# Kernel optimization log

Hardware: AMD Instinct MI355X
Metric: run time of the kernel (lower is better)

## Reference

```python
import jax, jax.numpy as jnp
import numpy as np

F = 4        # number of factors
M = 256      # codebook size per factor
D = 8192     # hypervector dimension
B = 256      # batch of composite vectors to factorize
ITERS = 10   # resonator iterations


def setup_inputs() -> dict:
    key = jax.random.key(0)
    k1, k2 = jax.random.split(key, 2)
    # bipolar (+1/-1) codebooks, shape [F, M, D]
    cb = jnp.sign(jax.random.normal(k1, (F, M, D), dtype=jnp.float32))
    codebooks = jnp.where(cb == 0, 1.0, cb)
    # composite inputs: bind (elementwise product) of one random codevector per factor
    idx = jax.random.randint(k2, (B, F), 0, M)                       # [B, F]
    chosen = codebooks[jnp.arange(F)[None, :], idx]                  # [B, F, D]
    inp = jnp.prod(chosen, axis=1)                                   # [B, D]
    return {"input": inp, "codebooks": codebooks}


def _stage_concurrent(inp, est, codebooks):
    # est: [B, F, D]; codebooks: [F, M, D]; inp: [B, D]
    n = est.shape[1]
    # inv_others[:, f] = prod_{j != f} est[:, j]  (bipolar inverse == identity)
    inv_others = jnp.stack(
        [jnp.prod(jnp.concatenate([est[:, :f], est[:, f + 1:]], axis=1), axis=1)
         for f in range(n)], axis=1)                                  # [B, F, D]
    new_est = inp[:, None, :] * inv_others                            # bind -> [B, F, D]
    sim = jnp.einsum('bfd,fmd->bfm', new_est, codebooks)              # similarity
    # activation == 'NONE'
    out = jnp.einsum('bfm,fmd->bfd', sim, codebooks)                  # dot_similarity
    return jnp.sign(out)


def reference(input, codebooks):
    Bn = input.shape[0]
    # init estimates = multiset (sum) of each codebook, broadcast over batch
    init = jnp.broadcast_to(jnp.sum(codebooks, axis=1)[None], (Bn, F, D)).astype(input.dtype)

    def cond(state):
        _, k, done = state
        return jnp.logical_and(k < ITERS, jnp.logical_not(done))

    def body(state):
        est, k, _ = state
        new = _stage_concurrent(input, est, codebooks)
        return (new, k + 1, jnp.all(new == est))

    est, k, _ = jax.lax.while_loop(cond, body, (init, jnp.int32(0), jnp.array(False)))
    # cleanup: nearest codevector per factor (argmax similarity)
    sim = jnp.einsum('bfd,fmd->bfm', est, codebooks)
    outcome = jnp.argmax(sim, axis=-1)                                # [B, F] indices
    return outcome, k
```

## Files before the change

### kernel.cpp

```cpp
#include <hip/hip_runtime.h>

#define B_SZ 256
#define F_SZ 4
#define M_SZ 256
#define D_SZ 8192
#define NITER 10

typedef signed char i8;
typedef unsigned long long u64;
typedef signed char c16 __attribute__((ext_vector_type(16)));
typedef int v4i __attribute__((ext_vector_type(4)));

#define NBFM (B_SZ * F_SZ * M_SZ)

#define OFF_CB    ((size_t)0)
#define OFF_CBT   ((size_t)8  << 20)
#define OFF_IN8   ((size_t)16 << 20)
#define OFF_CBBT  ((size_t)18 << 20)
#define OFF_INB   ((size_t)19 << 20)
#define OFF_ESB   ((size_t)20 << 20)
#define OFF_EZB   ((size_t)21 << 20)
#define OFF_SIMX  ((size_t)22 << 20)
#define OFF_P1    ((size_t)23 << 20)
#define OFF_S32   ((size_t)48 << 20)
#define OFF_PDIG  (OFF_S32 + (size_t)F_SZ * D_SZ * 4)
#define OFF_CHG   (OFF_PDIG + (size_t)3 * F_SZ * D_SZ)


__global__ __launch_bounds__(256) void k_cvt_cb(const float* __restrict__ src,
                                                i8* __restrict__ cb, i8* __restrict__ cbt) {
  __shared__ i8 tile[32][33];
  const int bid = blockIdx.x;
  const int f = bid >> 11;
  const int rem = bid & 2047;
  const int m0 = (rem >> 8) << 5;
  const int d0 = (rem & 255) << 5;
  const int t = threadIdx.x;
  const int i = t >> 3, j = (t & 7) << 2;
  const float4 v = *(const float4*)(src + ((size_t)(f * M_SZ + m0 + i)) * D_SZ + d0 + j);
  char4 c;
  c.x = v.x > 0.f ? 1 : -1;
  c.y = v.y > 0.f ? 1 : -1;
  c.z = v.z > 0.f ? 1 : -1;
  c.w = v.w > 0.f ? 1 : -1;
  *(char4*)(cb + ((size_t)(f * M_SZ + m0 + i)) * D_SZ + d0 + j) = c;
  tile[i][j + 0] = c.x; tile[i][j + 1] = c.y; tile[i][j + 2] = c.z; tile[i][j + 3] = c.w;
  __syncthreads();
  const int dd = t >> 3, jm = (t & 7) << 2;
  char4 o;
  o.x = tile[jm + 0][dd]; o.y = tile[jm + 1][dd]; o.z = tile[jm + 2][dd]; o.w = tile[jm + 3][dd];
  *(char4*)(cbt + ((size_t)(f * D_SZ + d0 + dd)) * M_SZ + m0 + jm) = o;
}

__global__ __launch_bounds__(256) void k_cvt_in(const float* __restrict__ src, i8* __restrict__ dst) {
  const int idx = blockIdx.x * 256 + threadIdx.x;
  const float4 v = ((const float4*)src)[idx];
  char4 c;
  c.x = v.x > 0.f ? 1 : -1;
  c.y = v.y > 0.f ? 1 : -1;
  c.z = v.z > 0.f ? 1 : -1;
  c.w = v.w > 0.f ? 1 : -1;
  ((char4*)dst)[idx] = c;
}

__global__ __launch_bounds__(256) void k_pack_cb(const i8* __restrict__ cb, u64* __restrict__ cbbT) {
  const int id = blockIdx.x * 256 + threadIdx.x;
  const int f = id >> 15;
  const int rem = id & 32767;
  const int w = rem >> 8;
  const int m = rem & 255;
  const i8* src = cb + ((size_t)(f * M_SZ + m)) * D_SZ + w * 64;
  u64 r = 0;
  #pragma unroll
  for (int k = 0; k < 4; ++k) {
    c16 v = *(const c16*)(src + k * 16);
    u64 part = 0;
    #pragma unroll
    for (int j = 0; j < 16; ++j) part |= ((u64)(((unsigned char)v[j]) >> 7)) << j;
    r |= part << (k * 16);
  }
  cbbT[((size_t)(f * 128 + w)) * 256 + m] = r;
}

__global__ __launch_bounds__(256) void k_pack_in(const i8* __restrict__ in8, u64* __restrict__ inb) {
  const int id = blockIdx.x * 256 + threadIdx.x;
  const int b = id >> 7;
  const int w = id & 127;
  const i8* src = in8 + (size_t)b * D_SZ + w * 64;
  u64 r = 0;
  #pragma unroll
  for (int k = 0; k < 4; ++k) {
    c16 v = *(const c16*)(src + k * 16);
    u64 part = 0;
    #pragma unroll
    for (int j = 0; j < 16; ++j) part |= ((u64)(((unsigned char)v[j]) >> 7)) << j;
    r |= part << (k * 16);
  }
  inb[(size_t)b * 128 + w] = r;
}

__global__ __launch_bounds__(256) void k_S(const i8* __restrict__ cb, int* __restrict__ S) {
  const int id = blockIdx.x * 256 + threadIdx.x;
  const int f = id >> 13, d = id & 8191;
  const i8* p = cb + (size_t)f * M_SZ * D_SZ + d;
  int s = 0;
  for (int m = 0; m < M_SZ; ++m) s += p[(size_t)m * D_SZ];
  S[id] = s;
}

__global__ __launch_bounds__(256) void k_P(const int* __restrict__ S, i8* __restrict__ pdig) {
  const int d = blockIdx.x * 256 + threadIdx.x;
  const int s0 = S[d], s1 = S[D_SZ + d], s2 = S[2 * D_SZ + d], s3 = S[3 * D_SZ + d];
  int P[4];
  P[0] = s1 * s2 * s3;
  P[1] = s0 * s2 * s3;
  P[2] = s0 * s1 * s3;
  P[3] = s0 * s1 * s2;
  for (int f = 0; f < 4; ++f) {
    int x = P[f] >> 3;
    #pragma unroll
    for (int p = 0; p < 2; ++p) {
      const int y = x + 127;
      const int q = (y >= 0) ? (y / 255) : -((-y + 254) / 255);
      const int dg = x - q * 255;
      pdig[((size_t)(p * F_SZ + f)) * D_SZ + d] = (i8)dg;
      x = q;
    }
    pdig[((size_t)(2 * F_SZ + f)) * D_SZ + d] = (i8)x;
  }
}


__global__ __launch_bounds__(256) void ga2_kernel(
    const i8* __restrict__ in8, const i8* __restrict__ cb,
    const i8* __restrict__ pdig, int* __restrict__ p1)
{
  __shared__ __align__(16) i8 lA[64 * 48];
  __shared__ __align__(16) i8 lB[128 * 48];

  const int bid = blockIdx.x;
  const int s = bid & 7;
  const int r = bid >> 3;
  const int p = r % 3;
  const int q = r / 3;
  const int f = q & 3;
  const int ct = q >> 2;
  const int b0 = (ct >> 1) * 64;
  const int m0 = (ct & 1) * 128;
  const int ksteps = 32;
  const int kbase = s << 10;

  const int t = threadIdx.x;
  const int lane = t & 63;
  const int wv = t >> 6;
  const int wrow = (wv >> 1) * 32;
  const int wcol = (wv & 1) * 64;

  const int arow = t >> 1;
  const int aoff = (t & 1) * 16;
  const i8* pB  = cb   + ((size_t)(f * M_SZ + m0 + arow)) * D_SZ + aoff;
  const i8* pDg = pdig + ((size_t)(p * F_SZ + f)) * D_SZ + aoff;
  const i8* pIn = in8  + (size_t)(b0 + arow) * D_SZ + aoff;

  v4i acc[2][4];
  #pragma unroll
  for (int tr = 0; tr < 2; ++tr)
    #pragma unroll
    for (int tc = 0; tc < 4; ++tc) acc[tr][tc] = 0;

  c16 va = 0, vb = 0;
  {
    const int kk = kbase;
    vb = (*(const c16*)(pB + kk)) * (*(const c16*)(pDg + kk));
    if (t < 128) va = *(const c16*)(pIn + kk);
  }

  for (int j = 0; j < ksteps; ++j) {
    c16 sa = va, sb = vb;
    if (j + 1 < ksteps) {
      const int kk = kbase + (j + 1) * 32;
      vb = (*(const c16*)(pB + kk)) * (*(const c16*)(pDg + kk));
      if (t < 128) va = *(const c16*)(pIn + kk);
    }
    __syncthreads();
    if (t < 128) *(c16*)&lA[arow * 48 + aoff] = sa;
    *(c16*)&lB[arow * 48 + aoff] = sb;
    __syncthreads();

    const int rsel = lane & 15;
    const int kq = (lane >> 4) * 8;
    long af[2], bf[4];
    #pragma unroll
    for (int tr = 0; tr < 2; ++tr) af[tr] = *(const long*)&lA[(wrow + tr * 16 + rsel) * 48 + kq];
    #pragma unroll
    for (int tc = 0; tc < 4; ++tc) bf[tc] = *(const long*)&lB[(wcol + tc * 16 + rsel) * 48 + kq];
    #pragma unroll
    for (int tr = 0; tr < 2; ++tr)
      #pragma unroll
      for (int tc = 0; tc < 4; ++tc)
        acc[tr][tc] = __builtin_amdgcn_mfma_i32_16x16x32_i8(af[tr], bf[tc], acc[tr][tc], 0, 0, 0);
  }

  const int colb = lane & 15;
  const int rowq = (lane >> 4) * 4;
  const size_t obase = (size_t)(p * 8 + s) * NBFM;
  #pragma unroll
  for (int tr = 0; tr < 2; ++tr)
    #pragma unroll
    for (int tc = 0; tc < 4; ++tc)
      #pragma unroll
      for (int rr = 0; rr < 4; ++rr) {
        const int b = b0 + wrow + tr * 16 + rowq + rr;
        const int m = m0 + wcol + tc * 16 + colb;
        p1[obase + (((size_t)(b * F_SZ + f)) << 8) + m] = acc[tr][tc][rr];
      }
}

__global__ __launch_bounds__(256) void k_digits1(const int* __restrict__ p1, i8* __restrict__ simx) {
  const int idx = blockIdx.x * 256 + threadIdx.x;
  long long g[3];
  #pragma unroll
  for (int p = 0; p < 3; ++p) {
    long long gg = 0;
    #pragma unroll
    for (int s = 0; s < 8; ++s) gg += (long long)p1[(size_t)(p * 8 + s) * NBFM + idx];
    g[p] = gg;
  }
  const long long sim = g[0] + 255LL * g[1] + 65025LL * g[2];
  int x = (int)sim;
  const int r1 = (x + 128) >> 8;
  const int d0 = x - (r1 << 8);
  const int r2 = (r1 + 128) >> 8;
  const int d1 = r1 - (r2 << 8);
  const size_t bf = (size_t)(idx >> 8);
  const int m = idx & 255;
  simx[bf * 768 + m] = (i8)d0;
  simx[bf * 768 + 256 + m] = (i8)d1;
  simx[bf * 768 + 512 + m] = (i8)r2;
}


__global__ __launch_bounds__(256) void ga_bit(
    const u64* __restrict__ esb, const u64* __restrict__ ezb,
    const u64* __restrict__ inb, const u64* __restrict__ cbbT,
    i8* __restrict__ simx, const int* __restrict__ changed, int it)
{
  __shared__ u64 AL[128][4];
  __shared__ int C0[2];

  if (changed[it - 1] == 0) return;

  const int bid = blockIdx.x;
  const int f = bid & 3;
  const int b0 = (bid >> 2) * 2;
  const int t = threadIdx.x;
  if (t < 2) C0[t] = 0;
  __syncthreads();

  {
    const int r = t >> 7, w = t & 127;
    const int b = b0 + r;
    int ffs[3]; int c = 0;
    for (int ff = 0; ff < 4; ++ff) if (ff != f) ffs[c++] = ff;
    const size_t base = (size_t)b * 4 * 128;
    const u64 s = inb[(size_t)b * 128 + w]
      ^ esb[base + ffs[0] * 128 + w] ^ esb[base + ffs[1] * 128 + w] ^ esb[base + ffs[2] * 128 + w];
    const u64 nz = ~(ezb[base + ffs[0] * 128 + w] | ezb[base + ffs[1] * 128 + w] | ezb[base + ffs[2] * 128 + w]);
    AL[w][r * 2] = s;
    AL[w][r * 2 + 1] = nz;
    int pcv = (int)__popcll(nz);
    #pragma unroll
    for (int off = 32; off >= 1; off >>= 1) pcv += __shfl_down(pcv, off);
    if ((t & 63) == 0) atomicAdd(&C0[r], pcv);
  }
  __syncthreads();

  const int m = t;
  int a0 = 0, a1 = 0;
  const u64* pc = cbbT + (size_t)f * 128 * 256 + m;
  #pragma unroll 4
  for (int w = 0; w < 128; ++w) {
    const u64 cbw = pc[w * 256];
    const u64 s0 = AL[w][0], z0 = AL[w][1], s1 = AL[w][2], z1 = AL[w][3];
    a0 += (int)__popcll((s0 ^ cbw) & z0);
    a1 += (int)__popcll((s1 ^ cbw) & z1);
  }
  const int sim0 = C0[0] - 2 * a0;
  const int sim1 = C0[1] - 2 * a1;

  int d1 = (sim0 + 128) >> 8; int d0v = sim0 - (d1 << 8);
  const size_t bf0 = ((size_t)b0 * 4 + f) * 768;
  simx[bf0 + m] = (i8)d0v; simx[bf0 + 256 + m] = (i8)d1;
  d1 = (sim1 + 128) >> 8; d0v = sim1 - (d1 << 8);
  const size_t bf1 = ((size_t)(b0 + 1) * 4 + f) * 768;
  simx[bf1 + m] = (i8)d0v; simx[bf1 + 256 + m] = (i8)d1;
}


template<int NP, bool FIRST>
__global__ __launch_bounds__(256) void gb_kernel(
    const i8* __restrict__ simx, const i8* __restrict__ cbt,
    u64* __restrict__ esb, u64* __restrict__ ezb,
    const int* __restrict__ S32,
    int* __restrict__ changed, int it)
{
  __shared__ __align__(16) i8 lB[8 * 8 * 64 * 8];
  __shared__ int chgf;

  if (!FIRST) { if (changed[it - 1] == 0) return; }

  const int bid = blockIdx.x;
  const int f = bid & 3;
  const int ct = bid >> 2;
  const int b0 = (ct >> 6) * 64;
  const int d0 = (ct & 63) * 128;

  const int t = threadIdx.x;
  if (t == 0) chgf = 0;
  const int lane = t & 63;
  const int wv = t >> 6;
  const int wrow = (wv >> 1) * 32;
  const int wcol = (wv & 1) * 64;

  {
    const int c = t & 15;
    const int dr0 = t >> 4;
    const int ks = c >> 1;
    const int q0 = (c & 1) * 2;
    #pragma unroll
    for (int i = 0; i < 8; ++i) {
      const int dr = dr0 + i * 16;
      union { c16 v; u64 u[2]; } x;
      x.v = *(const c16*)(cbt + ((size_t)(f * D_SZ + d0 + dr)) * M_SZ + c * 16);
      const int tile = dr >> 4;
      const int col = dr & 15;
      *(u64*)&lB[((((ks * 8 + tile) * 4 + q0) * 16 + col)) * 8] = x.u[0];
      *(u64*)&lB[((((ks * 8 + tile) * 4 + q0 + 1) * 16 + col)) * 8] = x.u[1];
    }
  }
  __syncthreads();

  v4i acc[NP][2][4];
  #pragma unroll
  for (int pp = 0; pp < NP; ++pp)
    #pragma unroll
    for (int tr = 0; tr < 2; ++tr)
      #pragma unroll
      for (int tc = 0; tc < 4; ++tc) acc[pp][tr][tc] = 0;

  const int rsel = lane & 15;
  const int kq = (lane >> 4) * 8;
  const int tb = wcol >> 4;

  #pragma unroll
  for (int ks = 0; ks < 8; ++ks) {
    long bf[4];
    #pragma unroll
    for (int tc = 0; tc < 4; ++tc)
      bf[tc] = *(const long*)&lB[((ks * 8 + tb + tc) * 64 + lane) * 8];
    #pragma unroll
    for (int pp = 0; pp < NP; ++pp) {
      long af[2];
      #pragma unroll
      for (int tr = 0; tr < 2; ++tr) {
        const int row = b0 + wrow + tr * 16 + rsel;
        af[tr] = *(const long*)(simx + ((size_t)(row * 4 + f)) * 768 + pp * 256 + ks * 32 + kq);
      }
      #pragma unroll
      for (int tr = 0; tr < 2; ++tr)
        #pragma unroll
        for (int tc = 0; tc < 4; ++tc)
          acc[pp][tr][tc] = __builtin_amdgcn_mfma_i32_16x16x32_i8(af[tr], bf[tc], acc[pp][tr][tc], 0, 0, 0);
    }
  }

  bool chl = false;
  const int colb = lane & 15;

  #pragma unroll
  for (int tr = 0; tr < 2; ++tr) {
    unsigned long long bs[4][4], bz[4][4];
    #pragma unroll
    for (int rr = 0; rr < 4; ++rr)
      #pragma unroll
      for (int tc = 0; tc < 4; ++tc) {
        int o = acc[0][tr][tc][rr];
        if (NP > 1) o += acc[1][tr][tc][rr] * 256;
        if (NP > 2) o += acc[2][tr][tc][rr] * 65536;
        bs[rr][tc] = __ballot(o < 0);
        bz[rr][tc] = __ballot(o == 0);
        if (FIRST) {
          const int sg = (o > 0) - (o < 0);
          const int d = d0 + wcol + tc * 16 + colb;
          chl |= (sg != S32[f * D_SZ + d]);
        }
      }
    u64 ws = 0, wz = 0;
    #pragma unroll
    for (int rl = 0; rl < 16; ++rl) {
      const int g = rl >> 2, rr = rl & 3;
      u64 vs = 0, vz = 0;
      #pragma unroll
      for (int tc = 0; tc < 4; ++tc) {
        vs |= ((bs[rr][tc] >> (g * 16)) & 0xFFFFull) << (tc * 16);
        vz |= ((bz[rr][tc] >> (g * 16)) & 0xFFFFull) << (tc * 16);
      }
      if (lane == rl) { ws = vs; wz = vz; }
    }
    if (lane < 16) {
      const int row = b0 + wrow + tr * 16 + lane;
      const size_t wi = ((size_t)(row * 4 + f)) * 128 + ((d0 + wcol) >> 6);
      if (!FIRST) chl |= (ws != esb[wi]) | (wz != ezb[wi]);
      esb[wi] = ws;
      ezb[wi] = wz;
    }
  }
  if (chl) atomicOr(&chgf, 1);
  __syncthreads();
  if (t == 0 && chgf) atomicOr(&changed[it], 1);
}


__global__ __launch_bounds__(256) void k_final(
    const u64* __restrict__ esb, const u64* __restrict__ ezb,
    const u64* __restrict__ cbbT, const int* __restrict__ chg,
    int* __restrict__ out)
{
  __shared__ u64 AL[128][4];
  __shared__ int C0[2];
  __shared__ long long red0[256], red1[256];

  const int bid = blockIdx.x;
  const int f = bid & 3;
  const int b0 = (bid >> 2) * 2;
  const int t = threadIdx.x;
  if (t < 2) C0[t] = 0;
  __syncthreads();

  {
    const int r = t >> 7, w = t & 127;
    const int b = b0 + r;
    const size_t a = ((size_t)b * 4 + f) * 128 + w;
    const u64 s = esb[a];
    const u64 nz = ~ezb[a];
    AL[w][r * 2] = s;
    AL[w][r * 2 + 1] = nz;
    int pcv = (int)__popcll(nz);
    #pragma unroll
    for (int off = 32; off >= 1; off >>= 1) pcv += __shfl_down(pcv, off);
    if ((t & 63) == 0) atomicAdd(&C0[r], pcv);
  }
  __syncthreads();

  const int m = t;
  int a0 = 0, a1 = 0;
  const u64* pc = cbbT + (size_t)f * 128 * 256 + m;
  #pragma unroll 4
  for (int w = 0; w < 128; ++w) {
    const u64 cbw = pc[w * 256];
    const u64 s0 = AL[w][0], z0 = AL[w][1], s1 = AL[w][2], z1 = AL[w][3];
    a0 += (int)__popcll((s0 ^ cbw) & z0);
    a1 += (int)__popcll((s1 ^ cbw) & z1);
  }
  const int sim0 = C0[0] - 2 * a0;
  const int sim1 = C0[1] - 2 * a1;

  red0[m] = ((long long)sim0 << 32) | (long long)(unsigned)(255 - m);
  red1[m] = ((long long)sim1 << 32) | (long long)(unsigned)(255 - m);
  __syncthreads();
  for (int s2 = 128; s2 > 0; s2 >>= 1) {
    if (m < s2) {
      if (red0[m + s2] > red0[m]) red0[m] = red0[m + s2];
      if (red1[m + s2] > red1[m]) red1[m] = red1[m + s2];
    }
    __syncthreads();
  }
  if (m == 0) {
    out[b0 * 4 + f] = 255 - (int)(red0[0] & 0xFFFF);
    out[(b0 + 1) * 4 + f] = 255 - (int)(red1[0] & 0xFFFF);
    if (bid == 0) {
      int k = NITER;
      for (int i = 1; i <= NITER; ++i) if (chg[i] == 0) { k = i; break; }
      out[B_SZ * F_SZ] = k;
    }
  }
}


extern "C" void kernel_launch(void* const* d_in, const int* in_sizes, int n_in,
                              void* d_out, int out_size, void* d_ws, size_t ws_size,
                              hipStream_t stream) {
  const float* f_in = (const float*)d_in[0];
  const float* f_cb = (const float*)d_in[1];
  int* out = (int*)d_out;
  char* ws = (char*)d_ws;

  i8*  cb8  = (i8*)(ws + OFF_CB);
  i8*  cbt8 = (i8*)(ws + OFF_CBT);
  i8*  in8  = (i8*)(ws + OFF_IN8);
  u64* cbbT = (u64*)(ws + OFF_CBBT);
  u64* inb  = (u64*)(ws + OFF_INB);
  u64* esb  = (u64*)(ws + OFF_ESB);
  u64* ezb  = (u64*)(ws + OFF_EZB);
  i8*  simx = (i8*)(ws + OFF_SIMX);
  int* p1   = (int*)(ws + OFF_P1);
  int* S32  = (int*)(ws + OFF_S32);
  i8*  pdig = (i8*)(ws + OFF_PDIG);
  int* chg  = (int*)(ws + OFF_CHG);

  hipMemsetAsync(chg, 0, 64, stream);
  k_cvt_cb<<<dim3(8192), dim3(256), 0, stream>>>(f_cb, cb8, cbt8);
  k_cvt_in<<<dim3(2048), dim3(256), 0, stream>>>(f_in, in8);
  k_pack_cb<<<dim3(512), dim3(256), 0, stream>>>(cb8, cbbT);
  k_pack_in<<<dim3(128), dim3(256), 0, stream>>>(in8, inb);
  k_S<<<dim3(128), dim3(256), 0, stream>>>(cb8, S32);
  k_P<<<dim3(32), dim3(256), 0, stream>>>(S32, pdig);

  ga2_kernel<<<dim3(768), dim3(256), 0, stream>>>(in8, cb8, pdig, p1);
  k_digits1<<<dim3(1024), dim3(256), 0, stream>>>(p1, simx);
  gb_kernel<3, true><<<dim3(1024), dim3(256), 0, stream>>>(
      simx, cbt8, esb, ezb, S32, chg, 1);

  for (int it = 2; it <= NITER; ++it) {
    ga_bit<<<dim3(512), dim3(256), 0, stream>>>(esb, ezb, inb, cbbT, simx, chg, it);
    gb_kernel<2, false><<<dim3(1024), dim3(256), 0, stream>>>(
        simx, cbt8, esb, ezb, nullptr, chg, it);
  }

  k_final<<<dim3(512), dim3(256), 0, stream>>>(esb, ezb, cbbT, chg, out);
}
```

Measured before the change: 565.1 us.

## Fuse prep kernels and run iterations in one persistent kernel with grid barriers

Merges the codebook conversion, transpose, bit-packing and column-sum into a single prep kernel (column sums accumulated with atomics), and does the same for the input. Iterations 2..N plus the final argmax run in one persistent 256-block kernel that syncs between phases with a software grid barrier, replacing about 20 small launches. Each block now processes several work units serially, so there is less parallelism per phase, and correctness relies on all 256 blocks being co-resident for the spin barrier.

Result: slower. 1.215 ms (+114.9%).

```diff
diff --git a/kernel.cpp b/kernel.cpp
--- a/kernel.cpp
+++ b/kernel.cpp
@@ -22,90 +22,97 @@
 #define OFF_EZB   ((size_t)21 << 20)
 #define OFF_SIMX  ((size_t)22 << 20)
 #define OFF_P1    ((size_t)23 << 20)
-#define OFF_S32   ((size_t)48 << 20)
-#define OFF_PDIG  (OFF_S32 + (size_t)F_SZ * D_SZ * 4)
-#define OFF_CHG   (OFF_PDIG + (size_t)3 * F_SZ * D_SZ)
-
-
-__global__ __launch_bounds__(256) void k_cvt_cb(const float* __restrict__ src,
-                                                i8* __restrict__ cb, i8* __restrict__ cbt) {
-  __shared__ i8 tile[32][33];
+#define OFF_S32   ((size_t)47 << 20)
+#define OFF_CHG   (OFF_S32 + (size_t)131072)
+#define OFF_BAR   (OFF_CHG + (size_t)64)
+#define OFF_PDIG  (OFF_BAR + (size_t)64)
+
+__device__ __forceinline__ u64 msk8(u64 x) {
+  return (((x >> 7) & 0x0101010101010101ull) * 0x0102040810204080ull) >> 56;
+}
+
+__device__ __forceinline__ void gridbar(int* bar, int t) {
+  __syncthreads();
+  if (t == 0) {
+    __threadfence();
+    const int g = __hip_atomic_load(&bar[1], __ATOMIC_RELAXED, __HIP_MEMORY_SCOPE_AGENT);
+    const int v = __hip_atomic_fetch_add(&bar[0], 1, __ATOMIC_ACQ_REL, __HIP_MEMORY_SCOPE_AGENT);
+    if (v == 255) {
+      __hip_atomic_store(&bar[0], 0, __ATOMIC_RELAXED, __HIP_MEMORY_SCOPE_AGENT);
+      __hip_atomic_fetch_add(&bar[1], 1, __ATOMIC_RELEASE, __HIP_MEMORY_SCOPE_AGENT);
+    } else {
+      while (__hip_atomic_load(&bar[1], __ATOMIC_ACQUIRE, __HIP_MEMORY_SCOPE_AGENT) == g)
+        __builtin_amdgcn_s_sleep(1);
+    }
+    __threadfence();
+  }
+  __syncthreads();
+}
+
+
+__global__ __launch_bounds__(256) void k_prep_cb(const float* __restrict__ src,
+                                                 i8* __restrict__ cb, i8* __restrict__ cbt,
+                                                 u64* __restrict__ cbbT, int* __restrict__ S32) {
+  __shared__ __align__(16) i8 tile[16][64];
   const int bid = blockIdx.x;
   const int f = bid >> 11;
-  const int rem = bid & 2047;
-  const int m0 = (rem >> 8) << 5;
-  const int d0 = (rem & 255) << 5;
+  const int mt = (bid >> 7) & 15;
+  const int dt = bid & 127;
+  const int m0 = mt * 16, d0 = dt * 64;
   const int t = threadIdx.x;
-  const int i = t >> 3, j = (t & 7) << 2;
-  const float4 v = *(const float4*)(src + ((size_t)(f * M_SZ + m0 + i)) * D_SZ + d0 + j);
-  char4 c;
-  c.x = v.x > 0.f ? 1 : -1;
-  c.y = v.y > 0.f ? 1 : -1;
-  c.z = v.z > 0.f ? 1 : -1;
-  c.w = v.w > 0.f ? 1 : -1;
-  *(char4*)(cb + ((size_t)(f * M_SZ + m0 + i)) * D_SZ + d0 + j) = c;
-  tile[i][j + 0] = c.x; tile[i][j + 1] = c.y; tile[i][j + 2] = c.z; tile[i][j + 3] = c.w;
+  const int mi = t >> 4, c = t & 15;
+  const float4 v = *(const float4*)(src + ((size_t)(f * M_SZ + m0 + mi)) * D_SZ + d0 + c * 4);
+  char4 cc;
+  cc.x = v.x > 0.f ? 1 : -1;
+  cc.y = v.y > 0.f ? 1 : -1;
+  cc.z = v.z > 0.f ? 1 : -1;
+  cc.w = v.w > 0.f ? 1 : -1;
+  *(char4*)(cb + ((size_t)(f * M_SZ + m0 + mi)) * D_SZ + d0 + c * 4) = cc;
+  *(char4*)&tile[mi][c * 4] = cc;
   __syncthreads();
-  const int dd = t >> 3, jm = (t & 7) << 2;
-  char4 o;
-  o.x = tile[jm + 0][dd]; o.y = tile[jm + 1][dd]; o.z = tile[jm + 2][dd]; o.w = tile[jm + 3][dd];
-  *(char4*)(cbt + ((size_t)(f * D_SZ + d0 + dd)) * M_SZ + m0 + jm) = o;
-}
-
-__global__ __launch_bounds__(256) void k_cvt_in(const float* __restrict__ src, i8* __restrict__ dst) {
-  const int idx = blockIdx.x * 256 + threadIdx.x;
-  const float4 v = ((const float4*)src)[idx];
-  char4 c;
-  c.x = v.x > 0.f ? 1 : -1;
-  c.y = v.y > 0.f ? 1 : -1;
-  c.z = v.z > 0.f ? 1 : -1;
-  c.w = v.w > 0.f ? 1 : -1;
-  ((char4*)dst)[idx] = c;
-}
-
-__global__ __launch_bounds__(256) void k_pack_cb(const i8* __restrict__ cb, u64* __restrict__ cbbT) {
-  const int id = blockIdx.x * 256 + threadIdx.x;
-  const int f = id >> 15;
-  const int rem = id & 32767;
-  const int w = rem >> 8;
-  const int m = rem & 255;
-  const i8* src = cb + ((size_t)(f * M_SZ + m)) * D_SZ + w * 64;
-  u64 r = 0;
-  #pragma unroll
-  for (int k = 0; k < 4; ++k) {
-    c16 v = *(const c16*)(src + k * 16);
-    u64 part = 0;
-    #pragma unroll
-    for (int j = 0; j < 16; ++j) part |= ((u64)(((unsigned char)v[j]) >> 7)) << j;
-    r |= part << (k * 16);
-  }
-  cbbT[((size_t)(f * 128 + w)) * 256 + m] = r;
-}
-
-__global__ __launch_bounds__(256) void k_pack_in(const i8* __restrict__ in8, u64* __restrict__ inb) {
-  const int id = blockIdx.x * 256 + threadIdx.x;
-  const int b = id >> 7;
-  const int w = id & 127;
-  const i8* src = in8 + (size_t)b * D_SZ + w * 64;
-  u64 r = 0;
-  #pragma unroll
-  for (int k = 0; k < 4; ++k) {
-    c16 v = *(const c16*)(src + k * 16);
-    u64 part = 0;
-    #pragma unroll
-    for (int j = 0; j < 16; ++j) part |= ((u64)(((unsigned char)v[j]) >> 7)) << j;
-    r |= part << (k * 16);
-  }
-  inb[(size_t)b * 128 + w] = r;
-}
-
-__global__ __launch_bounds__(256) void k_S(const i8* __restrict__ cb, int* __restrict__ S) {
-  const int id = blockIdx.x * 256 + threadIdx.x;
-  const int f = id >> 13, d = id & 8191;
-  const i8* p = cb + (size_t)f * M_SZ * D_SZ + d;
-  int s = 0;
-  for (int m = 0; m < M_SZ; ++m) s += p[(size_t)m * D_SZ];
-  S[id] = s;
+  if (t < 64) {
+    const int dd = t;
+    c16 o;
+    int ssum = 0;
+    #pragma unroll
+    for (int mm = 0; mm < 16; ++mm) { const i8 val = tile[mm][dd]; o[mm] = val; ssum += val; }
+    *(c16*)(cbt + ((size_t)(f * D_SZ + d0 + dd)) * M_SZ + m0) = o;
+    atomicAdd(&S32[f * D_SZ + d0 + dd], ssum);
+  } else if (t < 80) {
+    const int m = t - 64;
+    const u64* row = (const u64*)&tile[m][0];
+    u64 w = 0;
+    #pragma unroll
+    for (int j = 0; j < 8; ++j) w |= msk8(row[j]) << (8 * j);
+    cbbT[((size_t)(f * 128 + dt)) * 256 + (m0 + m)] = w;
+  }
+}
+
+__global__ __launch_bounds__(256) void k_prep_in(const float* __restrict__ src,
+                                                 i8* __restrict__ dst, u64* __restrict__ inb) {
+  __shared__ __align__(16) i8 tile[16][64];
+  const int bid = blockIdx.x;
+  const int bt = bid >> 7;
+  const int dt = bid & 127;
+  const int b0 = bt * 16, d0 = dt * 64;
+  const int t = threadIdx.x;
+  const int mi = t >> 4, c = t & 15;
+  const float4 v = *(const float4*)(src + ((size_t)(b0 + mi)) * D_SZ + d0 + c * 4);
+  char4 cc;
+  cc.x = v.x > 0.f ? 1 : -1;
+  cc.y = v.y > 0.f ? 1 : -1;
+  cc.z = v.z > 0.f ? 1 : -1;
+  cc.w = v.w > 0.f ? 1 : -1;
+  *(char4*)(dst + ((size_t)(b0 + mi)) * D_SZ + d0 + c * 4) = cc;
+  *(char4*)&tile[mi][c * 4] = cc;
+  __syncthreads();
+  if (t < 16) {
+    const u64* row = (const u64*)&tile[t][0];
+    u64 w = 0;
+    #pragma unroll
+    for (int j = 0; j < 8; ++j) w |= msk8(row[j]) << (8 * j);
+    inb[(size_t)(b0 + t) * 128 + dt] = w;
+  }
 }
 
 __global__ __launch_bounds__(256) void k_P(const int* __restrict__ S, i8* __restrict__ pdig) {
@@ -240,74 +247,13 @@
 }
 
 
-__global__ __launch_bounds__(256) void ga_bit(
-    const u64* __restrict__ esb, const u64* __restrict__ ezb,
-    const u64* __restrict__ inb, const u64* __restrict__ cbbT,
-    i8* __restrict__ simx, const int* __restrict__ changed, int it)
-{
-  __shared__ u64 AL[128][4];
-  __shared__ int C0[2];
-
-  if (changed[it - 1] == 0) return;
-
-  const int bid = blockIdx.x;
-  const int f = bid & 3;
-  const int b0 = (bid >> 2) * 2;
-  const int t = threadIdx.x;
-  if (t < 2) C0[t] = 0;
-  __syncthreads();
-
-  {
-    const int r = t >> 7, w = t & 127;
-    const int b = b0 + r;
-    int ffs[3]; int c = 0;
-    for (int ff = 0; ff < 4; ++ff) if (ff != f) ffs[c++] = ff;
-    const size_t base = (size_t)b * 4 * 128;
-    const u64 s = inb[(size_t)b * 128 + w]
-      ^ esb[base + ffs[0] * 128 + w] ^ esb[base + ffs[1] * 128 + w] ^ esb[base + ffs[2] * 128 + w];
-    const u64 nz = ~(ezb[base + ffs[0] * 128 + w] | ezb[base + ffs[1] * 128 + w] | ezb[base + ffs[2] * 128 + w]);
-    AL[w][r * 2] = s;
-    AL[w][r * 2 + 1] = nz;
-    int pcv = (int)__popcll(nz);
-    #pragma unroll
-    for (int off = 32; off >= 1; off >>= 1) pcv += __shfl_down(pcv, off);
-    if ((t & 63) == 0) atomicAdd(&C0[r], pcv);
-  }
-  __syncthreads();
-
-  const int m = t;
-  int a0 = 0, a1 = 0;
-  const u64* pc = cbbT + (size_t)f * 128 * 256 + m;
-  #pragma unroll 4
-  for (int w = 0; w < 128; ++w) {
-    const u64 cbw = pc[w * 256];
-    const u64 s0 = AL[w][0], z0 = AL[w][1], s1 = AL[w][2], z1 = AL[w][3];
-    a0 += (int)__popcll((s0 ^ cbw) & z0);
-    a1 += (int)__popcll((s1 ^ cbw) & z1);
-  }
-  const int sim0 = C0[0] - 2 * a0;
-  const int sim1 = C0[1] - 2 * a1;
-
-  int d1 = (sim0 + 128) >> 8; int d0v = sim0 - (d1 << 8);
-  const size_t bf0 = ((size_t)b0 * 4 + f) * 768;
-  simx[bf0 + m] = (i8)d0v; simx[bf0 + 256 + m] = (i8)d1;
-  d1 = (sim1 + 128) >> 8; d0v = sim1 - (d1 << 8);
-  const size_t bf1 = ((size_t)(b0 + 1) * 4 + f) * 768;
-  simx[bf1 + m] = (i8)d0v; simx[bf1 + 256 + m] = (i8)d1;
-}
-
-
-template<int NP, bool FIRST>
-__global__ __launch_bounds__(256) void gb_kernel(
+__global__ __launch_bounds__(256) void gb_first(
     const i8* __restrict__ simx, const i8* __restrict__ cbt,
     u64* __restrict__ esb, u64* __restrict__ ezb,
-    const int* __restrict__ S32,
-    int* __restrict__ changed, int it)
+    const int* __restrict__ S32, int* __restrict__ changed)
 {
   __shared__ __align__(16) i8 lB[8 * 8 * 64 * 8];
   __shared__ int chgf;
-
-  if (!FIRST) { if (changed[it - 1] == 0) return; }
 
   const int bid = blockIdx.x;
   const int f = bid & 3;
@@ -340,9 +286,9 @@
   }
   __syncthreads();
 
-  v4i acc[NP][2][4];
+  v4i acc[3][2][4];
   #pragma unroll
-  for (int pp = 0; pp < NP; ++pp)
+  for (int pp = 0; pp < 3; ++pp)
     #pragma unroll
     for (int tr = 0; tr < 2; ++tr)
       #pragma unroll
@@ -354,12 +300,12 @@
 
   #pragma unroll
   for (int ks = 0; ks < 8; ++ks) {
-    long bf[4];
+    long bfv[4];
     #pragma unroll
     for (int tc = 0; tc < 4; ++tc)
-      bf[tc] = *(const long*)&lB[((ks * 8 + tb + tc) * 64 + lane) * 8];
-    #pragma unroll
-    for (int pp = 0; pp < NP; ++pp) {
+      bfv[tc] = *(const long*)&lB[((ks * 8 + tb + tc) * 64 + lane) * 8];
+    #pragma unroll
+    for (int pp = 0; pp < 3; ++pp) {
       long af[2];
       #pragma unroll
       for (int tr = 0; tr < 2; ++tr) {
@@ -370,30 +316,25 @@
       for (int tr = 0; tr < 2; ++tr)
         #pragma unroll
         for (int tc = 0; tc < 4; ++tc)
-          acc[pp][tr][tc] = __builtin_amdgcn_mfma_i32_16x16x32_i8(af[tr], bf[tc], acc[pp][tr][tc], 0, 0, 0);
+          acc[pp][tr][tc] = __builtin_amdgcn_mfma_i32_16x16x32_i8(af[tr], bfv[tc], acc[pp][tr][tc], 0, 0, 0);
     }
   }
 
   bool chl = false;
   const int colb = lane & 15;
-
   #pragma unroll
   for (int tr = 0; tr < 2; ++tr) {
-    unsigned long long bs[4][4], bz[4][4];
+    u64 bs[4][4], bz[4][4];
     #pragma unroll
     for (int rr = 0; rr < 4; ++rr)
       #pragma unroll
       for (int tc = 0; tc < 4; ++tc) {
-        int o = acc[0][tr][tc][rr];
-        if (NP > 1) o += acc[1][tr][tc][rr] * 256;
-        if (NP > 2) o += acc[2][tr][tc][rr] * 65536;
+        int o = acc[0][tr][tc][rr] + acc[1][tr][tc][rr] * 256 + acc[2][tr][tc][rr] * 65536;
         bs[rr][tc] = __ballot(o < 0);
         bz[rr][tc] = __ballot(o == 0);
-        if (FIRST) {
-          const int sg = (o > 0) - (o < 0);
-          const int d = d0 + wcol + tc * 16 + colb;
-          chl |= (sg != S32[f * D_SZ + d]);
-        }
+        const int sg = (o > 0) - (o < 0);
+        const int d = d0 + wcol + tc * 16 + colb;
+        chl |= (sg != S32[f * D_SZ + d]);
       }
     u64 ws = 0, wz = 0;
     #pragma unroll
@@ -410,78 +351,243 @@
     if (lane < 16) {
       const int row = b0 + wrow + tr * 16 + lane;
       const size_t wi = ((size_t)(row * 4 + f)) * 128 + ((d0 + wcol) >> 6);
-      if (!FIRST) chl |= (ws != esb[wi]) | (wz != ezb[wi]);
       esb[wi] = ws;
       ezb[wi] = wz;
     }
   }
   if (chl) atomicOr(&chgf, 1);
   __syncthreads();
-  if (t == 0 && chgf) atomicOr(&changed[it], 1);
-}
-
-
-__global__ __launch_bounds__(256) void k_final(
-    const u64* __restrict__ esb, const u64* __restrict__ ezb,
-    const u64* __restrict__ cbbT, const int* __restrict__ chg,
-    int* __restrict__ out)
+  if (t == 0 && chgf) atomicOr(&changed[1], 1);
+}
+
+
+__global__ __launch_bounds__(256) void k_persist(
+    u64* __restrict__ esb, u64* __restrict__ ezb,
+    const u64* __restrict__ inb, const u64* __restrict__ cbbT,
+    const i8* __restrict__ cbt, i8* __restrict__ simx,
+    int* __restrict__ chg, int* __restrict__ bar, int* __restrict__ out)
 {
-  __shared__ u64 AL[128][4];
-  __shared__ int C0[2];
-  __shared__ long long red0[256], red1[256];
+  __shared__ __align__(16) i8 lS[32768];
+  __shared__ int chgf;
 
   const int bid = blockIdx.x;
-  const int f = bid & 3;
-  const int b0 = (bid >> 2) * 2;
   const int t = threadIdx.x;
-  if (t < 2) C0[t] = 0;
-  __syncthreads();
+  const int lane = t & 63;
+
+  for (int it = 2; it <= NITER; ++it) {
+    const bool active =
+        __hip_atomic_load(&chg[it - 1], __ATOMIC_RELAXED, __HIP_MEMORY_SCOPE_AGENT) != 0;
+
+    if (active) {
+      u64* AL = (u64*)lS;
+      int* C0 = (int*)(lS + 4096);
+      #pragma unroll 1
+      for (int u = 0; u < 2; ++u) {
+        const int unit = bid * 2 + u;
+        const int f = unit & 3;
+        const int b0 = (unit >> 2) * 2;
+        if (t < 2) C0[t] = 0;
+        __syncthreads();
+        {
+          const int r = t >> 7, w = t & 127;
+          const int b = b0 + r;
+          int ffs[3]; int c = 0;
+          for (int ff = 0; ff < 4; ++ff) if (ff != f) ffs[c++] = ff;
+          const size_t base = (size_t)b * 512;
+          const u64 s = inb[(size_t)b * 128 + w]
+            ^ esb[base + ffs[0] * 128 + w] ^ esb[base + ffs[1] * 128 + w] ^ esb[base + ffs[2] * 128 + w];
+          const u64 z = ~(ezb[base + ffs[0] * 128 + w] | ezb[base + ffs[1] * 128 + w] | ezb[base + ffs[2] * 128 + w]);
+          AL[w * 4 + r * 2] = s;
+          AL[w * 4 + r * 2 + 1] = z;
+          int pcv = (int)__popcll(z);
+          #pragma unroll
+          for (int off = 32; off >= 1; off >>= 1) pcv += __shfl_down(pcv, off);
+          if (lane == 0) atomicAdd(&C0[r], pcv);
+        }
+        __syncthreads();
+        int a0 = 0, a1 = 0;
+        const u64* pc = cbbT + (size_t)f * 32768 + t;
+        #pragma unroll 4
+        for (int w = 0; w < 128; ++w) {
+          const u64 cbw = pc[w * 256];
+          a0 += (int)__popcll((AL[w * 4 + 0] ^ cbw) & AL[w * 4 + 1]);
+          a1 += (int)__popcll((AL[w * 4 + 2] ^ cbw) & AL[w * 4 + 3]);
+        }
+        const int sim0 = C0[0] - 2 * a0;
+        const int sim1 = C0[1] - 2 * a1;
+        int d1 = (sim0 + 128) >> 8; int d0v = sim0 - (d1 << 8);
+        const size_t bf0 = ((size_t)b0 * 4 + f) * 768;
+        simx[bf0 + t] = (i8)d0v; simx[bf0 + 256 + t] = (i8)d1;
+        d1 = (sim1 + 128) >> 8; d0v = sim1 - (d1 << 8);
+        const size_t bf1 = ((size_t)(b0 + 1) * 4 + f) * 768;
+        simx[bf1 + t] = (i8)d0v; simx[bf1 + 256 + t] = (i8)d1;
+        __syncthreads();
+      }
+    }
+    gridbar(bar, t);
+
+    if (active) {
+      if (t == 0) chgf = 0;
+      bool chl = false;
+      #pragma unroll 1
+      for (int u = 0; u < 4; ++u) {
+        const int unit = bid * 4 + u;
+        const int f = unit & 3;
+        const int ct = unit >> 2;
+        const int b0 = (ct >> 6) * 64;
+        const int d0 = (ct & 63) * 128;
+        const int wv = t >> 6;
+        const int wrow = (wv >> 1) * 32;
+        const int wcol = (wv & 1) * 64;
+        {
+          const int c = t & 15;
+          const int dr0 = t >> 4;
+          const int ks = c >> 1;
+          const int q0 = (c & 1) * 2;
+          #pragma unroll
+          for (int i = 0; i < 8; ++i) {
+            const int dr = dr0 + i * 16;
+            union { c16 v; u64 uu[2]; } x;
+            x.v = *(const c16*)(cbt + ((size_t)(f * D_SZ + d0 + dr)) * M_SZ + c * 16);
+            const int tile = dr >> 4;
+            const int col = dr & 15;
+            *(u64*)&lS[((((ks * 8 + tile) * 4 + q0) * 16 + col)) * 8] = x.uu[0];
+            *(u64*)&lS[((((ks * 8 + tile) * 4 + q0 + 1) * 16 + col)) * 8] = x.uu[1];
+          }
+        }
+        __syncthreads();
+
+        v4i acc[2][2][4];
+        #pragma unroll
+        for (int pp = 0; pp < 2; ++pp)
+          #pragma unroll
+          for (int tr = 0; tr < 2; ++tr)
+            #pragma unroll
+            for (int tc = 0; tc < 4; ++tc) acc[pp][tr][tc] = 0;
+
+        const int rsel = lane & 15;
+        const int kq = (lane >> 4) * 8;
+        const int tb = wcol >> 4;
+
+        #pragma unroll
+        for (int ks = 0; ks < 8; ++ks) {
+          long bfv[4];
+          #pragma unroll
+          for (int tc = 0; tc < 4; ++tc)
+            bfv[tc] = *(const long*)&lS[((ks * 8 + tb + tc) * 64 + lane) * 8];
+          #pragma unroll
+          for (int pp = 0; pp < 2; ++pp) {
+            long af[2];
+            #pragma unroll
+            for (int tr = 0; tr < 2; ++tr) {
+              const int row = b0 + wrow + tr * 16 + rsel;
+              af[tr] = *(const long*)(simx + ((size_t)(row * 4 + f)) * 768 + pp * 256 + ks * 32 + kq);
+            }
+            #pragma unroll
+            for (int tr = 0; tr < 2; ++tr)
+              #pragma unroll
+              for (int tc = 0; tc < 4; ++tc)
+                acc[pp][tr][tc] = __builtin_amdgcn_mfma_i32_16x16x32_i8(af[tr], bfv[tc], acc[pp][tr][tc], 0, 0, 0);
+          }
+        }
+
+        #pragma unroll
+        for (int tr = 0; tr < 2; ++tr) {
+          u64 bs[4][4], bz[4][4];
+          #pragma unroll
+          for (int rr = 0; rr < 4; ++rr)
+            #pragma unroll
+            for (int tc = 0; tc < 4; ++tc) {
+              const int o = acc[0][tr][tc][rr] + acc[1][tr][tc][rr] * 256;
+              bs[rr][tc] = __ballot(o < 0);
+              bz[rr][tc] = __ballot(o == 0);
+            }
+          u64 ws = 0, wz = 0;
+          #pragma unroll
+          for (int rl = 0; rl < 16; ++rl) {
+            const int g = rl >> 2, rr = rl & 3;
+            u64 vs = 0, vz = 0;
+            #pragma unroll
+            for (int tc = 0; tc < 4; ++tc) {
+              vs |= ((bs[rr][tc] >> (g * 16)) & 0xFFFFull) << (tc * 16);
+              vz |= ((bz[rr][tc] >> (g * 16)) & 0xFFFFull) << (tc * 16);
+            }
+            if (lane == rl) { ws = vs; wz = vz; }
+          }
+          if (lane < 16) {
+            const int row = b0 + wrow + tr * 16 + lane;
+            const size_t wi = ((size_t)(row * 4 + f)) * 128 + ((d0 + wcol) >> 6);
+            chl |= (ws != esb[wi]) | (wz != ezb[wi]);
+            esb[wi] = ws;
+            ezb[wi] = wz;
+          }
+        }
+        __syncthreads();
+      }
+      if (chl) atomicOr(&chgf, 1);
+      __syncthreads();
+      if (t == 0 && chgf) atomicOr(&chg[it], 1);
+    }
+    gridbar(bar, t);
+  }
 
   {
-    const int r = t >> 7, w = t & 127;
-    const int b = b0 + r;
-    const size_t a = ((size_t)b * 4 + f) * 128 + w;
-    const u64 s = esb[a];
-    const u64 nz = ~ezb[a];
-    AL[w][r * 2] = s;
-    AL[w][r * 2 + 1] = nz;
-    int pcv = (int)__popcll(nz);
-    #pragma unroll
-    for (int off = 32; off >= 1; off >>= 1) pcv += __shfl_down(pcv, off);
-    if ((t & 63) == 0) atomicAdd(&C0[r], pcv);
-  }
-  __syncthreads();
-
-  const int m = t;
-  int a0 = 0, a1 = 0;
-  const u64* pc = cbbT + (size_t)f * 128 * 256 + m;
-  #pragma unroll 4
-  for (int w = 0; w < 128; ++w) {
-    const u64 cbw = pc[w * 256];
-    const u64 s0 = AL[w][0], z0 = AL[w][1], s1 = AL[w][2], z1 = AL[w][3];
-    a0 += (int)__popcll((s0 ^ cbw) & z0);
-    a1 += (int)__popcll((s1 ^ cbw) & z1);
-  }
-  const int sim0 = C0[0] - 2 * a0;
-  const int sim1 = C0[1] - 2 * a1;
-
-  red0[m] = ((long long)sim0 << 32) | (long long)(unsigned)(255 - m);
-  red1[m] = ((long long)sim1 << 32) | (long long)(unsigned)(255 - m);
-  __syncthreads();
-  for (int s2 = 128; s2 > 0; s2 >>= 1) {
-    if (m < s2) {
-      if (red0[m + s2] > red0[m]) red0[m] = red0[m + s2];
-      if (red1[m + s2] > red1[m]) red1[m] = red1[m + s2];
-    }
-    __syncthreads();
-  }
-  if (m == 0) {
-    out[b0 * 4 + f] = 255 - (int)(red0[0] & 0xFFFF);
-    out[(b0 + 1) * 4 + f] = 255 - (int)(red1[0] & 0xFFFF);
-    if (bid == 0) {
-      int k = NITER;
-      for (int i = 1; i <= NITER; ++i) if (chg[i] == 0) { k = i; break; }
-      out[B_SZ * F_SZ] = k;
+    u64* AL = (u64*)lS;
+    int* C0 = (int*)(lS + 4096);
+    long long* red0 = (long long*)(lS + 4224);
+    long long* red1 = (long long*)(lS + 6272);
+    #pragma unroll 1
+    for (int u = 0; u < 2; ++u) {
+      const int unit = bid * 2 + u;
+      const int f = unit & 3;
+      const int b0 = (unit >> 2) * 2;
+      if (t < 2) C0[t] = 0;
+      __syncthreads();
+      {
+        const int r = t >> 7, w = t & 127;
+        const int b = b0 + r;
+        const size_t a = ((size_t)b * 4 + f) * 128 + w;
+        const u64 s = esb[a];
+        const u64 z = ~ezb[a];
+        AL[w * 4 + r * 2] = s;
+        AL[w * 4 + r * 2 + 1] = z;
+        int pcv = (int)__popcll(z);
+        #pragma unroll
+        for (int off = 32; off >= 1; off >>= 1) pcv += __shfl_down(pcv, off);
+        if (lane == 0) atomicAdd(&C0[r], pcv);
+      }
+      __syncthreads();
+      int a0 = 0, a1 = 0;
+      const u64* pc = cbbT + (size_t)f * 32768 + t;
+      #pragma unroll 4
+      for (int w = 0; w < 128; ++w) {
+        const u64 cbw = pc[w * 256];
+        a0 += (int)__popcll((AL[w * 4 + 0] ^ cbw) & AL[w * 4 + 1]);
+        a1 += (int)__popcll((AL[w * 4 + 2] ^ cbw) & AL[w * 4 + 3]);
+      }
+      const int sim0 = C0[0] - 2 * a0;
+      const int sim1 = C0[1] - 2 * a1;
+      red0[t] = ((long long)sim0 << 32) | (long long)(unsigned)(255 - t);
+      red1[t] = ((long long)sim1 << 32) | (long long)(unsigned)(255 - t);
+      __syncthreads();
+      for (int s2 = 128; s2 > 0; s2 >>= 1) {
+        if (t < s2) {
+          if (red0[t + s2] > red0[t]) red0[t] = red0[t + s2];
+          if (red1[t + s2] > red1[t]) red1[t] = red1[t + s2];
+        }
+        __syncthreads();
+      }
+      if (t == 0) {
+        out[b0 * 4 + f] = 255 - (int)(red0[0] & 0xFFFF);
+        out[(b0 + 1) * 4 + f] = 255 - (int)(red1[0] & 0xFFFF);
+        if (unit == 0) {
+          int k = NITER;
+          for (int i = 1; i <= NITER; ++i)
+            if (__hip_atomic_load(&chg[i], __ATOMIC_RELAXED, __HIP_MEMORY_SCOPE_AGENT) == 0) { k = i; break; }
+          out[B_SZ * F_SZ] = k;
+        }
+      }
+      __syncthreads();
     }
   }
 }
@@ -505,27 +611,18 @@
   i8*  simx = (i8*)(ws + OFF_SIMX);
   int* p1   = (int*)(ws + OFF_P1);
   int* S32  = (int*)(ws + OFF_S32);
+  int* chg  = (int*)(ws + OFF_CHG);
+  int* bar  = (int*)(ws + OFF_BAR);
   i8*  pdig = (i8*)(ws + OFF_PDIG);
-  int* chg  = (int*)(ws + OFF_CHG);
-
-  hipMemsetAsync(chg, 0, 64, stream);
-  k_cvt_cb<<<dim3(8192), dim3(256), 0, stream>>>(f_cb, cb8, cbt8);
-  k_cvt_in<<<dim3(2048), dim3(256), 0, stream>>>(f_in, in8);
-  k_pack_cb<<<dim3(512), dim3(256), 0, stream>>>(cb8, cbbT);
-  k_pack_in<<<dim3(128), dim3(256), 0, stream>>>(in8, inb);
-  k_S<<<dim3(128), dim3(256), 0, stream>>>(cb8, S32);
+
+  hipMemsetAsync(ws + OFF_S32, 0, 131072 + 128, stream);
+  k_prep_cb<<<dim3(8192), dim3(256), 0, stream>>>(f_cb, cb8, cbt8, cbbT, S32);
+  k_prep_in<<<dim3(2048), dim3(256), 0, stream>>>(f_in, in8, inb);
   k_P<<<dim3(32), dim3(256), 0, stream>>>(S32, pdig);
 
   ga2_kernel<<<dim3(768), dim3(256), 0, stream>>>(in8, cb8, pdig, p1);
   k_digits1<<<dim3(1024), dim3(256), 0, stream>>>(p1, simx);
-  gb_kernel<3, true><<<dim3(1024), dim3(256), 0, stream>>>(
-      simx, cbt8, esb, ezb, S32, chg, 1);
-
-  for (int it = 2; it <= NITER; ++it) {
-    ga_bit<<<dim3(512), dim3(256), 0, stream>>>(esb, ezb, inb, cbbT, simx, chg, it);
-    gb_kernel<2, false><<<dim3(1024), dim3(256), 0, stream>>>(
-        simx, cbt8, esb, ezb, nullptr, chg, it);
-  }
-
-  k_final<<<dim3(512), dim3(256), 0, stream>>>(esb, ezb, cbbT, chg, out);
-}
+  gb_first<<<dim3(1024), dim3(256), 0, stream>>>(simx, cbt8, esb, ezb, S32, chg);
+
+  k_persist<<<dim3(256), dim3(256), 0, stream>>>(esb, ezb, inb, cbbT, cbt8, simx, chg, bar, out);
+}
```
